# Optimization experiments

Measured on AMD Instinct MI355X. Metric: run time of the kernel, lower is better.

The kernel has to match this reference:

```python
import jax, jax.numpy as jnp
import numpy as np

B, T, D = 2, 2048, 1024   # batch, seq, d_model
E, K, H = 8, 2, 704       # routed experts, topk, expert hidden
SH = 704 * 2              # shared-expert hidden = moe_hidden * num_shared_experts
EPS = 1e-20               # topk_norm_epsilon
STD = 0.02                # init_weight_std


def setup_inputs() -> dict:
    key = jax.random.key(0)
    ks = jax.random.split(key, 8)
    return {
        "x":   jax.random.normal(ks[0], (B, T, D), jnp.float32),
        "Wg":  jax.random.normal(ks[1], (E, D), jnp.float32) * STD,   # router experts_weights
        "W1":  jax.random.normal(ks[2], (E, D, H), jnp.float32) * STD,  # gate proj per expert
        "W3":  jax.random.normal(ks[3], (E, D, H), jnp.float32) * STD,  # up proj per expert
        "W2":  jax.random.normal(ks[4], (E, H, D), jnp.float32) * STD,  # down proj per expert
        "Ws1": jax.random.normal(ks[5], (D, SH), jnp.float32) * STD,    # shared expert
        "Ws3": jax.random.normal(ks[6], (D, SH), jnp.float32) * STD,
        "Ws2": jax.random.normal(ks[7], (SH, D), jnp.float32) * STD,
    }


def reference(x, Wg, W1, W3, W2, Ws1, Ws3, Ws2):
    b, t, d = x.shape
    n = b * t
    xf = x.reshape(n, d)
    # softmax gating + topk + scatter back into dense [N,E] gate matrix
    gates = jax.nn.softmax(xf @ Wg.T, axis=-1)                      # [N,E]
    top_v, top_i = jax.lax.top_k(gates, K)                          # [N,K]
    masked = jnp.zeros_like(gates).at[jnp.arange(n)[:, None], top_i].set(top_v)
    masked = masked / (masked.sum(-1, keepdims=True) + EPS)         # normalized_moe_gates
    # per-expert SwiGLU FFN over all tokens, then gate-weighted combine
    h = jnp.einsum('nd,edh->enh', xf, W1)                           # [E,N,H]
    g = jnp.einsum('nd,edh->enh', xf, W3)
    y = jnp.einsum('enh,ehd->end', jax.nn.silu(h) * g, W2)          # [E,N,D]
    routed = jnp.einsum('ne,end->nd', masked, y)                    # combine
    shared = (jax.nn.silu(xf @ Ws1) * (xf @ Ws3)) @ Ws2             # shared experts
    return (routed + shared).reshape(b, t, d)
```

## Files before the change

### kernel.cpp

```cpp
#include <hip/hip_runtime.h>
#include <math.h>

typedef __bf16 bf16;
typedef __attribute__((ext_vector_type(8))) __bf16 bf16x8;
typedef __attribute__((ext_vector_type(4))) __bf16 bf16x4;
typedef __attribute__((ext_vector_type(4))) float f32x4;

#define NTOK 4096
#define DM   1024
#define NE   8
#define HE   704
#define HS   1408

#define OFF_CNT   0u
#define OFF_TOK   256u
#define OFF_WGT   131328u
#define OFF_XB    262400u
#define OFF_W1T   8651008u
#define OFF_W3T   20185344u
#define OFF_W2T   31719680u
#define OFF_WS1T  43254016u
#define OFF_WS3T  46137600u
#define OFF_WS2T  49021184u
#define OFF_ACTR  51904768u
#define OFF_ACTS  63439104u
#define OFF_EIDS  74973440u
#define OFF_GW    74989824u

__global__ void cvt_x_kernel(const float* __restrict__ x, bf16* __restrict__ xb, int n4)
{
    int i = blockIdx.x * blockDim.x + threadIdx.x;
    if (i >= n4) return;
    float4 v = ((const float4*)x)[i];
    bf16x4 o;
    o[0] = (bf16)v.x; o[1] = (bf16)v.y; o[2] = (bf16)v.z; o[3] = (bf16)v.w;
    ((bf16x4*)xb)[i] = o;
}

__global__ void transpose_cvt(const float* __restrict__ src, bf16* __restrict__ dst, int R, int C)
{
    __shared__ float t[32][33];
    int c0 = blockIdx.x * 32, r0 = blockIdx.y * 32;
    size_t base = (size_t)blockIdx.z * (size_t)R * (size_t)C;
    src += base; dst += base;
    int row  = threadIdx.x >> 3;
    int col4 = (threadIdx.x & 7) * 4;
    float4 v = *(const float4*)&src[(size_t)(r0 + row) * C + c0 + col4];
    t[row][col4 + 0] = v.x; t[row][col4 + 1] = v.y;
    t[row][col4 + 2] = v.z; t[row][col4 + 3] = v.w;
    __syncthreads();
    bf16x4 o;
    o[0] = (bf16)t[col4 + 0][row];
    o[1] = (bf16)t[col4 + 1][row];
    o[2] = (bf16)t[col4 + 2][row];
    o[3] = (bf16)t[col4 + 3][row];
    *(bf16x4*)&dst[(size_t)(c0 + row) * R + r0 + col4] = o;
}

__global__ __launch_bounds__(256) void router_logits(
    const float* __restrict__ x, const float* __restrict__ Wg,
    int* __restrict__ eids, float2* __restrict__ gw)
{
    int n    = blockIdx.x * 4 + (threadIdx.x >> 6);
    int lane = threadIdx.x & 63;
    const float* xrow = x + (size_t)n * DM;
    float xr[16];
    #pragma unroll
    for (int j = 0; j < 16; j++) xr[j] = xrow[lane + 64 * j];
    float logit[NE];
    #pragma unroll
    for (int e = 0; e < NE; e++) {
        const float* wr = Wg + e * DM;
        float s = 0.f;
        #pragma unroll
        for (int j = 0; j < 16; j++) s += xr[j] * wr[lane + 64 * j];
        #pragma unroll
        for (int off = 32; off; off >>= 1) s += __shfl_xor(s, off, 64);
        logit[e] = s;
    }
    if (lane == 0) {
        int i0 = 0;
        #pragma unroll
        for (int e = 1; e < NE; e++) if (logit[e] > logit[i0]) i0 = e;
        int i1 = (i0 == 0) ? 1 : 0;
        #pragma unroll
        for (int e = 0; e < NE; e++) if (e != i0 && logit[e] > logit[i1]) i1 = e;
        float m = logit[0];
        #pragma unroll
        for (int e = 1; e < NE; e++) m = fmaxf(m, logit[e]);
        float denom = 0.f;
        #pragma unroll
        for (int e = 0; e < NE; e++) denom += expf(logit[e] - m);
        float g0 = expf(logit[i0] - m) / denom;
        float g1 = expf(logit[i1] - m) / denom;
        float inv = 1.f / (g0 + g1 + 1e-20f);
        eids[n] = i0 | (i1 << 16);
        gw[n] = make_float2(g0 * inv, g1 * inv);
    }
}

__global__ __launch_bounds__(128) void build_lists(
    const int* __restrict__ eids, const float2* __restrict__ gw,
    int* __restrict__ cnt, int* __restrict__ tok, float* __restrict__ wgt)
{
    __shared__ int lcnt[NE];
    __shared__ int gbase[NE];
    int t = threadIdx.x;
    int n = blockIdx.x * 128 + t;
    if (t < NE) lcnt[t] = 0;
    __syncthreads();
    int packed = eids[n];
    float2 w = gw[n];
    int e0 = packed & 0xffff, e1 = packed >> 16;
    int s0 = atomicAdd(&lcnt[e0], 1);
    int s1 = atomicAdd(&lcnt[e1], 1);
    __syncthreads();
    if (t < NE) gbase[t] = atomicAdd(&cnt[t], lcnt[t]);
    __syncthreads();
    int p0 = gbase[e0] + s0, p1 = gbase[e1] + s1;
    tok[e0 * NTOK + p0] = n; wgt[e0 * NTOK + p0] = w.x;
    tok[e1 * NTOK + p1] = n; wgt[e1 * NTOK + p1] = w.y;
}

__global__ void prefix_kernel(const int* __restrict__ cnt, int* __restrict__ pfx)
{
    if (threadIdx.x == 0) {
        int s = 0;
        for (int e = 0; e < NE; e++) { pfx[e] = s; s += cnt[e]; }
        pfx[NE] = s;
    }
}

__global__ __launch_bounds__(256) void gemm1_swiglu(
    const bf16* __restrict__ xb,
    const bf16* __restrict__ W1t, const bf16* __restrict__ W3t,
    bf16* __restrict__ act,
    const int* __restrict__ cnt, const int* __restrict__ pfx, const int* __restrict__ tok,
    int Hdim)
{
    int e = blockIdx.z;
    int count = cnt ? cnt[e] : NTOK;
    int m0 = blockIdx.y * 64;
    if (m0 >= count) return;
    int h0 = blockIdx.x * 64;
    int base = pfx ? pfx[e] : 0;
    const bf16* B1 = W1t + (size_t)e * Hdim * DM;
    const bf16* B3 = W3t + (size_t)e * Hdim * DM;
    const int* tlist = tok ? tok + e * NTOK : nullptr;

    __shared__ bf16 As[64][40];
    __shared__ bf16 Bs1[64][40];
    __shared__ bf16 Bs3[64][40];

    int tid  = threadIdx.x;
    int lrow = tid >> 2;
    int lcol = (tid & 3) * 8;

    int slot = m0 + lrow;
    int rowIdx;
    if (tlist) rowIdx = (slot < count) ? tlist[slot] : 0;
    else       rowIdx = (slot < count) ? slot : 0;
    const bf16* aPtr  = xb + (size_t)rowIdx * DM + lcol;
    const bf16* b1Ptr = B1 + (size_t)(h0 + lrow) * DM + lcol;
    const bf16* b3Ptr = B3 + (size_t)(h0 + lrow) * DM + lcol;

    int wv = tid >> 6, lane = tid & 63;
    int lm = lane & 15, lk = (lane >> 4) * 8;

    f32x4 acch[4], accg[4];
    #pragma unroll
    for (int c = 0; c < 4; c++) {
        acch[c] = (f32x4){0.f, 0.f, 0.f, 0.f};
        accg[c] = (f32x4){0.f, 0.f, 0.f, 0.f};
    }

    for (int k0 = 0; k0 < DM; k0 += 32) {
        *(uint4*)&As[lrow][lcol]  = *(const uint4*)(aPtr + k0);
        *(uint4*)&Bs1[lrow][lcol] = *(const uint4*)(b1Ptr + k0);
        *(uint4*)&Bs3[lrow][lcol] = *(const uint4*)(b3Ptr + k0);
        __syncthreads();
        bf16x8 af = *(const bf16x8*)&As[wv * 16 + lm][lk];
        #pragma unroll
        for (int c = 0; c < 4; c++) {
            bf16x8 b1f = *(const bf16x8*)&Bs1[c * 16 + lm][lk];
            bf16x8 b3f = *(const bf16x8*)&Bs3[c * 16 + lm][lk];
            acch[c] = __builtin_amdgcn_mfma_f32_16x16x32_bf16(af, b1f, acch[c], 0, 0, 0);
            accg[c] = __builtin_amdgcn_mfma_f32_16x16x32_bf16(af, b3f, accg[c], 0, 0, 0);
        }
        __syncthreads();
    }

    #pragma unroll
    for (int c = 0; c < 4; c++) {
        #pragma unroll
        for (int r = 0; r < 4; r++) {
            int row = wv * 16 + (lane >> 4) * 4 + r;
            int s2 = m0 + row;
            if (s2 < count) {
                float hv = acch[c][r], gv = accg[c][r];
                float a = hv / (1.f + expf(-hv)) * gv;
                act[(size_t)(base + s2) * Hdim + h0 + c * 16 + lm] = (bf16)a;
            }
        }
    }
}

__global__ __launch_bounds__(256) void gemm2_combine(
    const bf16* __restrict__ act,
    const bf16* __restrict__ W2t,
    float* __restrict__ out,
    const int* __restrict__ cnt, const int* __restrict__ pfx,
    const int* __restrict__ tok, const float* __restrict__ wgt,
    int Hdim, int atomic_mode)
{
    int e = blockIdx.z;
    int count = cnt ? cnt[e] : NTOK;
    int m0 = blockIdx.y * 64;
    if (m0 >= count) return;
    int d0 = blockIdx.x * 64;
    int base = pfx ? pfx[e] : 0;
    const bf16* B = W2t + (size_t)e * DM * Hdim;

    __shared__ bf16 As[64][40];
    __shared__ bf16 Bs[64][40];

    int tid  = threadIdx.x;
    int lrow = tid >> 2;
    int lcol = (tid & 3) * 8;

    int slot = m0 + lrow;
    int arow = (slot < count) ? (base + slot) : base;
    const bf16* aPtr = act + (size_t)arow * Hdim + lcol;
    const bf16* bPtr = B + (size_t)(d0 + lrow) * Hdim + lcol;

    int wv = tid >> 6, lane = tid & 63;
    int lm = lane & 15, lk = (lane >> 4) * 8;

    f32x4 acc[4];
    #pragma unroll
    for (int c = 0; c < 4; c++) acc[c] = (f32x4){0.f, 0.f, 0.f, 0.f};

    for (int k0 = 0; k0 < Hdim; k0 += 32) {
        *(uint4*)&As[lrow][lcol] = *(const uint4*)(aPtr + k0);
        *(uint4*)&Bs[lrow][lcol] = *(const uint4*)(bPtr + k0);
        __syncthreads();
        bf16x8 af = *(const bf16x8*)&As[wv * 16 + lm][lk];
        #pragma unroll
        for (int c = 0; c < 4; c++) {
            bf16x8 bf_ = *(const bf16x8*)&Bs[c * 16 + lm][lk];
            acc[c] = __builtin_amdgcn_mfma_f32_16x16x32_bf16(af, bf_, acc[c], 0, 0, 0);
        }
        __syncthreads();
    }

    #pragma unroll
    for (int c = 0; c < 4; c++) {
        #pragma unroll
        for (int r = 0; r < 4; r++) {
            int row = wv * 16 + (lane >> 4) * 4 + r;
            int s2 = m0 + row;
            if (s2 < count) {
                int col = d0 + c * 16 + lm;
                float v = acc[c][r];
                if (atomic_mode) {
                    int t = tok[e * NTOK + s2];
                    float w = wgt[e * NTOK + s2];
                    atomicAdd(&out[(size_t)t * DM + col], w * v);
                } else {
                    out[(size_t)s2 * DM + col] = v;
                }
            }
        }
    }
}

extern "C" void kernel_launch(void* const* d_in, const int* in_sizes, int n_in,
                              void* d_out, int out_size, void* d_ws, size_t ws_size,
                              hipStream_t stream)
{
    const float* x   = (const float*)d_in[0];
    const float* Wg  = (const float*)d_in[1];
    const float* W1  = (const float*)d_in[2];
    const float* W3  = (const float*)d_in[3];
    const float* W2  = (const float*)d_in[4];
    const float* Ws1 = (const float*)d_in[5];
    const float* Ws3 = (const float*)d_in[6];
    const float* Ws2 = (const float*)d_in[7];
    float* out = (float*)d_out;
    char*  ws  = (char*)d_ws;

    int*    cnt  = (int*)(ws + OFF_CNT);
    int*    pfx  = (int*)(ws + OFF_CNT + 32);
    int*    tok  = (int*)(ws + OFF_TOK);
    float*  wgt  = (float*)(ws + OFF_WGT);
    bf16*   xb   = (bf16*)(ws + OFF_XB);
    bf16*   w1t  = (bf16*)(ws + OFF_W1T);
    bf16*   w3t  = (bf16*)(ws + OFF_W3T);
    bf16*   w2t  = (bf16*)(ws + OFF_W2T);
    bf16*   ws1t = (bf16*)(ws + OFF_WS1T);
    bf16*   ws3t = (bf16*)(ws + OFF_WS3T);
    bf16*   ws2t = (bf16*)(ws + OFF_WS2T);
    bf16*   actr = (bf16*)(ws + OFF_ACTR);
    bf16*   acts = (bf16*)(ws + OFF_ACTS);
    int*    eids = (int*)(ws + OFF_EIDS);
    float2* gw   = (float2*)(ws + OFF_GW);

    hipMemsetAsync(ws, 0, 256, stream);

    cvt_x_kernel<<<4096, 256, 0, stream>>>(x, xb, NTOK * DM / 4);

    transpose_cvt<<<dim3(22, 32, 8), 256, 0, stream>>>(W1,  w1t,  1024, 704);
    transpose_cvt<<<dim3(22, 32, 8), 256, 0, stream>>>(W3,  w3t,  1024, 704);
    transpose_cvt<<<dim3(32, 22, 8), 256, 0, stream>>>(W2,  w2t,  704, 1024);
    transpose_cvt<<<dim3(44, 32, 1), 256, 0, stream>>>(Ws1, ws1t, 1024, 1408);
    transpose_cvt<<<dim3(44, 32, 1), 256, 0, stream>>>(Ws3, ws3t, 1024, 1408);
    transpose_cvt<<<dim3(32, 44, 1), 256, 0, stream>>>(Ws2, ws2t, 1408, 1024);

    router_logits<<<1024, 256, 0, stream>>>(x, Wg, eids, gw);
    build_lists<<<32, 128, 0, stream>>>(eids, gw, cnt, tok, wgt);
    prefix_kernel<<<1, 64, 0, stream>>>(cnt, pfx);

    gemm1_swiglu<<<dim3(HE / 64, 64, NE), 256, 0, stream>>>(xb, w1t, w3t, actr, cnt, pfx, tok, HE);
    gemm1_swiglu<<<dim3(HS / 64, 64, 1), 256, 0, stream>>>(xb, ws1t, ws3t, acts, nullptr, nullptr, nullptr, HS);
    gemm2_combine<<<dim3(DM / 64, 64, 1), 256, 0, stream>>>(acts, ws2t, out, nullptr, nullptr, nullptr, nullptr, HS, 0);
    gemm2_combine<<<dim3(DM / 64, 64, NE), 256, 0, stream>>>(actr, w2t, out, cnt, pfx, tok, wgt, HE, 1);
}
```

Before: 381.0 us.

## Enlarge GEMM tiles and stage loads via direct global-to-LDS copies

```diff
diff --git a/kernel.cpp b/kernel.cpp
--- a/kernel.cpp
+++ b/kernel.cpp
@@ -26,6 +26,13 @@
 #define OFF_ACTS  63439104u
 #define OFF_EIDS  74973440u
 #define OFF_GW    74989824u
+
+__device__ __forceinline__ void async_cp16(const bf16* g, bf16* l)
+{
+    __builtin_amdgcn_global_load_lds(
+        (const __attribute__((address_space(1))) unsigned int*)g,
+        (__attribute__((address_space(3))) unsigned int*)l, 16, 0, 0);
+}
 
 __global__ void cvt_x_kernel(const float* __restrict__ x, bf16* __restrict__ xb, int n4)
 {
@@ -140,7 +147,7 @@
 {
     int e = blockIdx.z;
     int count = cnt ? cnt[e] : NTOK;
-    int m0 = blockIdx.y * 64;
+    int m0 = blockIdx.y * 128;
     if (m0 >= count) return;
     int h0 = blockIdx.x * 64;
     int base = pfx ? pfx[e] : 0;
@@ -148,61 +155,79 @@
     const bf16* B3 = W3t + (size_t)e * Hdim * DM;
     const int* tlist = tok ? tok + e * NTOK : nullptr;
 
-    __shared__ bf16 As[64][40];
-    __shared__ bf16 Bs1[64][40];
-    __shared__ bf16 Bs3[64][40];
-
-    int tid  = threadIdx.x;
-    int lrow = tid >> 2;
-    int lcol = (tid & 3) * 8;
-
-    int slot = m0 + lrow;
-    int rowIdx;
-    if (tlist) rowIdx = (slot < count) ? tlist[slot] : 0;
-    else       rowIdx = (slot < count) ? slot : 0;
-    const bf16* aPtr  = xb + (size_t)rowIdx * DM + lcol;
-    const bf16* b1Ptr = B1 + (size_t)(h0 + lrow) * DM + lcol;
-    const bf16* b3Ptr = B3 + (size_t)(h0 + lrow) * DM + lcol;
-
-    int wv = tid >> 6, lane = tid & 63;
+    __shared__ bf16 As[128 * 32];
+    __shared__ bf16 B1s[64 * 32];
+    __shared__ bf16 B3s[64 * 32];
+
+    int tid = threadIdx.x, w = tid >> 6, lane = tid & 63;
+    int lrow4 = lane >> 2;
+    int lcol8 = (lane & 3) * 8;
+
+    int sA0 = m0 + 32 * w + lrow4;
+    int sA1 = sA0 + 16;
+    int rA0 = tlist ? (sA0 < count ? tlist[sA0] : 0) : (sA0 < count ? sA0 : 0);
+    int rA1 = tlist ? (sA1 < count ? tlist[sA1] : 0) : (sA1 < count ? sA1 : 0);
+    const bf16* ga0 = xb + (size_t)rA0 * DM + lcol8;
+    const bf16* ga1 = xb + (size_t)rA1 * DM + lcol8;
+    const bf16* gb1 = B1 + (size_t)(h0 + 16 * w + lrow4) * DM + lcol8;
+    const bf16* gb3 = B3 + (size_t)(h0 + 16 * w + lrow4) * DM + lcol8;
+    bf16* lA0 = As + 1024 * w;
+    bf16* lA1 = As + 1024 * w + 512;
+    bf16* lB1 = B1s + 512 * w;
+    bf16* lB3 = B3s + 512 * w;
+
+    int wm = (w & 1) * 64, wn = (w >> 1) * 32;
     int lm = lane & 15, lk = (lane >> 4) * 8;
 
-    f32x4 acch[4], accg[4];
-    #pragma unroll
-    for (int c = 0; c < 4; c++) {
-        acch[c] = (f32x4){0.f, 0.f, 0.f, 0.f};
-        accg[c] = (f32x4){0.f, 0.f, 0.f, 0.f};
-    }
+    f32x4 acch[4][2], accg[4][2];
+    #pragma unroll
+    for (int i = 0; i < 4; i++)
+        #pragma unroll
+        for (int j = 0; j < 2; j++) {
+            acch[i][j] = (f32x4){0.f, 0.f, 0.f, 0.f};
+            accg[i][j] = (f32x4){0.f, 0.f, 0.f, 0.f};
+        }
 
     for (int k0 = 0; k0 < DM; k0 += 32) {
-        *(uint4*)&As[lrow][lcol]  = *(const uint4*)(aPtr + k0);
-        *(uint4*)&Bs1[lrow][lcol] = *(const uint4*)(b1Ptr + k0);
-        *(uint4*)&Bs3[lrow][lcol] = *(const uint4*)(b3Ptr + k0);
+        async_cp16(ga0, lA0);
+        async_cp16(ga1, lA1);
+        async_cp16(gb1, lB1);
+        async_cp16(gb3, lB3);
+        ga0 += 32; ga1 += 32; gb1 += 32; gb3 += 32;
         __syncthreads();
-        bf16x8 af = *(const bf16x8*)&As[wv * 16 + lm][lk];
-        #pragma unroll
-        for (int c = 0; c < 4; c++) {
-            bf16x8 b1f = *(const bf16x8*)&Bs1[c * 16 + lm][lk];
-            bf16x8 b3f = *(const bf16x8*)&Bs3[c * 16 + lm][lk];
-            acch[c] = __builtin_amdgcn_mfma_f32_16x16x32_bf16(af, b1f, acch[c], 0, 0, 0);
-            accg[c] = __builtin_amdgcn_mfma_f32_16x16x32_bf16(af, b3f, accg[c], 0, 0, 0);
+        bf16x8 af[4], b1f[2], b3f[2];
+        #pragma unroll
+        for (int i = 0; i < 4; i++) af[i] = *(const bf16x8*)&As[(wm + i * 16 + lm) * 32 + lk];
+        #pragma unroll
+        for (int j = 0; j < 2; j++) {
+            b1f[j] = *(const bf16x8*)&B1s[(wn + j * 16 + lm) * 32 + lk];
+            b3f[j] = *(const bf16x8*)&B3s[(wn + j * 16 + lm) * 32 + lk];
         }
+        #pragma unroll
+        for (int i = 0; i < 4; i++)
+            #pragma unroll
+            for (int j = 0; j < 2; j++) {
+                acch[i][j] = __builtin_amdgcn_mfma_f32_16x16x32_bf16(af[i], b1f[j], acch[i][j], 0, 0, 0);
+                accg[i][j] = __builtin_amdgcn_mfma_f32_16x16x32_bf16(af[i], b3f[j], accg[i][j], 0, 0, 0);
+            }
         __syncthreads();
     }
 
-    #pragma unroll
-    for (int c = 0; c < 4; c++) {
-        #pragma unroll
-        for (int r = 0; r < 4; r++) {
-            int row = wv * 16 + (lane >> 4) * 4 + r;
-            int s2 = m0 + row;
-            if (s2 < count) {
-                float hv = acch[c][r], gv = accg[c][r];
-                float a = hv / (1.f + expf(-hv)) * gv;
-                act[(size_t)(base + s2) * Hdim + h0 + c * 16 + lm] = (bf16)a;
+    int quad = lane >> 4;
+    #pragma unroll
+    for (int i = 0; i < 4; i++)
+        #pragma unroll
+        for (int j = 0; j < 2; j++)
+            #pragma unroll
+            for (int r = 0; r < 4; r++) {
+                int row = wm + i * 16 + quad * 4 + r;
+                int s2 = m0 + row;
+                if (s2 < count) {
+                    float hv = acch[i][j][r], gv = accg[i][j][r];
+                    float a = hv / (1.f + expf(-hv)) * gv;
+                    act[(size_t)(base + s2) * Hdim + h0 + wn + j * 16 + lm] = (bf16)a;
+                }
             }
-        }
-    }
 }
 
 __global__ __launch_bounds__(256) void gemm2_combine(
@@ -215,63 +240,82 @@
 {
     int e = blockIdx.z;
     int count = cnt ? cnt[e] : NTOK;
-    int m0 = blockIdx.y * 64;
+    int m0 = blockIdx.y * 128;
     if (m0 >= count) return;
-    int d0 = blockIdx.x * 64;
+    int d0 = blockIdx.x * 128;
     int base = pfx ? pfx[e] : 0;
     const bf16* B = W2t + (size_t)e * DM * Hdim;
 
-    __shared__ bf16 As[64][40];
-    __shared__ bf16 Bs[64][40];
-
-    int tid  = threadIdx.x;
-    int lrow = tid >> 2;
-    int lcol = (tid & 3) * 8;
-
-    int slot = m0 + lrow;
-    int arow = (slot < count) ? (base + slot) : base;
-    const bf16* aPtr = act + (size_t)arow * Hdim + lcol;
-    const bf16* bPtr = B + (size_t)(d0 + lrow) * Hdim + lcol;
-
-    int wv = tid >> 6, lane = tid & 63;
+    __shared__ bf16 As[128 * 32];
+    __shared__ bf16 Bs[128 * 32];
+
+    int tid = threadIdx.x, w = tid >> 6, lane = tid & 63;
+    int lrow4 = lane >> 2;
+    int lcol8 = (lane & 3) * 8;
+
+    int sA0 = m0 + 32 * w + lrow4;
+    int sA1 = sA0 + 16;
+    int arow0 = (sA0 < count) ? (base + sA0) : base;
+    int arow1 = (sA1 < count) ? (base + sA1) : base;
+    const bf16* ga0 = act + (size_t)arow0 * Hdim + lcol8;
+    const bf16* ga1 = act + (size_t)arow1 * Hdim + lcol8;
+    const bf16* gb0 = B + (size_t)(d0 + 32 * w + lrow4) * Hdim + lcol8;
+    const bf16* gb1 = gb0 + (size_t)16 * Hdim;
+    bf16* lA0 = As + 1024 * w;
+    bf16* lA1 = As + 1024 * w + 512;
+    bf16* lB0 = Bs + 1024 * w;
+    bf16* lB1 = Bs + 1024 * w + 512;
+
+    int wm = (w & 1) * 64, wn = (w >> 1) * 64;
     int lm = lane & 15, lk = (lane >> 4) * 8;
 
-    f32x4 acc[4];
-    #pragma unroll
-    for (int c = 0; c < 4; c++) acc[c] = (f32x4){0.f, 0.f, 0.f, 0.f};
+    f32x4 acc[4][4];
+    #pragma unroll
+    for (int i = 0; i < 4; i++)
+        #pragma unroll
+        for (int j = 0; j < 4; j++) acc[i][j] = (f32x4){0.f, 0.f, 0.f, 0.f};
 
     for (int k0 = 0; k0 < Hdim; k0 += 32) {
-        *(uint4*)&As[lrow][lcol] = *(const uint4*)(aPtr + k0);
-        *(uint4*)&Bs[lrow][lcol] = *(const uint4*)(bPtr + k0);
+        async_cp16(ga0, lA0);
+        async_cp16(ga1, lA1);
+        async_cp16(gb0, lB0);
+        async_cp16(gb1, lB1);
+        ga0 += 32; ga1 += 32; gb0 += 32; gb1 += 32;
         __syncthreads();
-        bf16x8 af = *(const bf16x8*)&As[wv * 16 + lm][lk];
-        #pragma unroll
-        for (int c = 0; c < 4; c++) {
-            bf16x8 bf_ = *(const bf16x8*)&Bs[c * 16 + lm][lk];
-            acc[c] = __builtin_amdgcn_mfma_f32_16x16x32_bf16(af, bf_, acc[c], 0, 0, 0);
-        }
+        bf16x8 af[4], bf_[4];
+        #pragma unroll
+        for (int i = 0; i < 4; i++) af[i]  = *(const bf16x8*)&As[(wm + i * 16 + lm) * 32 + lk];
+        #pragma unroll
+        for (int j = 0; j < 4; j++) bf_[j] = *(const bf16x8*)&Bs[(wn + j * 16 + lm) * 32 + lk];
+        #pragma unroll
+        for (int i = 0; i < 4; i++)
+            #pragma unroll
+            for (int j = 0; j < 4; j++)
+                acc[i][j] = __builtin_amdgcn_mfma_f32_16x16x32_bf16(af[i], bf_[j], acc[i][j], 0, 0, 0);
         __syncthreads();
     }
 
-    #pragma unroll
-    for (int c = 0; c < 4; c++) {
-        #pragma unroll
-        for (int r = 0; r < 4; r++) {
-            int row = wv * 16 + (lane >> 4) * 4 + r;
-            int s2 = m0 + row;
-            if (s2 < count) {
-                int col = d0 + c * 16 + lm;
-                float v = acc[c][r];
-                if (atomic_mode) {
-                    int t = tok[e * NTOK + s2];
-                    float w = wgt[e * NTOK + s2];
-                    atomicAdd(&out[(size_t)t * DM + col], w * v);
-                } else {
-                    out[(size_t)s2 * DM + col] = v;
+    int quad = lane >> 4;
+    #pragma unroll
+    for (int i = 0; i < 4; i++)
+        #pragma unroll
+        for (int j = 0; j < 4; j++)
+            #pragma unroll
+            for (int r = 0; r < 4; r++) {
+                int row = wm + i * 16 + quad * 4 + r;
+                int s2 = m0 + row;
+                if (s2 < count) {
+                    int col = d0 + wn + j * 16 + lm;
+                    float v = acc[i][j][r];
+                    if (atomic_mode) {
+                        int t = tok[e * NTOK + s2];
+                        float wt = wgt[e * NTOK + s2];
+                        atomicAdd(&out[(size_t)t * DM + col], wt * v);
+                    } else {
+                        out[(size_t)s2 * DM + col] = v;
+                    }
                 }
             }
-        }
-    }
 }
 
 extern "C" void kernel_launch(void* const* d_in, const int* in_sizes, int n_in,
@@ -320,8 +364,8 @@
     build_lists<<<32, 128, 0, stream>>>(eids, gw, cnt, tok, wgt);
     prefix_kernel<<<1, 64, 0, stream>>>(cnt, pfx);
 
-    gemm1_swiglu<<<dim3(HE / 64, 64, NE), 256, 0, stream>>>(xb, w1t, w3t, actr, cnt, pfx, tok, HE);
-    gemm1_swiglu<<<dim3(HS / 64, 64, 1), 256, 0, stream>>>(xb, ws1t, ws3t, acts, nullptr, nullptr, nullptr, HS);
-    gemm2_combine<<<dim3(DM / 64, 64, 1), 256, 0, stream>>>(acts, ws2t, out, nullptr, nullptr, nullptr, nullptr, HS, 0);
-    gemm2_combine<<<dim3(DM / 64, 64, NE), 256, 0, stream>>>(actr, w2t, out, cnt, pfx, tok, wgt, HE, 1);
-}
+    gemm1_swiglu<<<dim3(HE / 64, 32, NE), 256, 0, stream>>>(xb, w1t, w3t, actr, cnt, pfx, tok, HE);
+    gemm1_swiglu<<<dim3(HS / 64, 32, 1), 256, 0, stream>>>(xb, ws1t, ws3t, acts, nullptr, nullptr, nullptr, HS);
+    gemm2_combine<<<dim3(DM / 128, 32, 1), 256, 0, stream>>>(acts, ws2t, out, nullptr, nullptr, nullptr, nullptr, HS, 0);
+    gemm2_combine<<<dim3(DM / 128, 32, NE), 256, 0, stream>>>(actr, w2t, out, cnt, pfx, tok, wgt, HE, 1);
+}
```

Result: faster. 367.5 us (-3.5%).
